# Optimization experiments

Measured on AMD Instinct MI355X. Metric: run time of the kernel, lower is better.

Reference implementation:

```python
import jax, jax.numpy as jnp
from jax import lax
import numpy as np


def conv2d(x, w, pad):
    # x: NCHW, w: OIHW
    return lax.conv_general_dilated(x, w, (1, 1), [(pad, pad), (pad, pad)],
                                    dimension_numbers=("NCHW", "OIHW", "NCHW"))


def make_dct_dict(num_atoms, num_dims):
    i = np.arange(num_atoms)[:, None].astype(np.float64)
    n = np.arange(num_dims)[None, :].astype(np.float64)
    w = np.cos((2.0 * n + 1.0) * i * (np.pi / (2.0 * num_dims)))
    w = w / np.linalg.norm(w, axis=1, keepdims=True)
    return jnp.asarray(w.T, dtype=jnp.float32)  # [num_dims, num_atoms]


def setup_inputs() -> dict:
    key = jax.random.key(0)
    B, C, H, W = 8, 64, 64, 64      # C = num_dims
    A = 256                          # num_atoms
    ks = jax.random.split(key, 10)
    s = 0.05
    Dict = make_dct_dict(A, C)       # [C, A]
    L = jnp.sum(Dict ** 2)           # ||Dict||_F^2 (scalar parameter)
    return {
        "x": jax.random.normal(ks[0], (B, C, H, W), jnp.float32),
        "conv_w": jax.random.normal(ks[1], (A, C, 3, 3), jnp.float32) * s,
        "conv_b": jax.random.normal(ks[2], (A,), jnp.float32) * s,
        "res1_w1": jax.random.normal(ks[3], (A // 2, A, 3, 3), jnp.float32) * s,
        "res1_w2": jax.random.normal(ks[4], (A, A // 2, 1, 1), jnp.float32) * s,
        "res2_w1": jax.random.normal(ks[5], (A // 2, A, 3, 3), jnp.float32) * s,
        "res2_w2": jax.random.normal(ks[6], (A, A // 2, 1, 1), jnp.float32) * s,
        "ca_w1": jax.random.normal(ks[7], (A // 16, A), jnp.float32) * s,  # Linear(A, A//16)
        "ca_w2": jax.random.normal(ks[8], (A, A // 16), jnp.float32) * s,  # Linear(A//16, A)
        "sa_w": jax.random.normal(ks[9], (1, 2, 3, 3), jnp.float32) * s,
        "Dict": Dict,
        "L": L,
        "num_iters": 16,
    }


def reference(x, conv_w, conv_b, res1_w1, res1_w2, res2_w1, res2_w2,
              ca_w1, ca_w2, sa_w, Dict, L, num_iters):
    def res_block(h, w1, w2):
        t = conv2d(jax.nn.relu(h), w1, 1)
        t = conv2d(jax.nn.relu(t), w2, 0)
        return h + t

    l = conv2d(x, conv_w, 1) + conv_b[None, :, None, None]
    l = res_block(l, res1_w1, res1_w2)
    l = res_block(l, res2_w1, res2_w2)

    # CBAM: channel attention (shared MLP on avg/max pooled features)
    avg = jnp.mean(l, axis=(2, 3))  # [B, A]
    mx = jnp.max(l, axis=(2, 3))
    fc = lambda v: jax.nn.relu(v @ ca_w1.T) @ ca_w2.T
    l = l * jax.nn.sigmoid(fc(avg) + fc(mx))[:, :, None, None]
    # CBAM: spatial attention
    s2 = jnp.concatenate([jnp.mean(l, axis=1, keepdims=True),
                          jnp.max(l, axis=1, keepdims=True)], axis=1)  # [B,2,H,W]
    l = l * jax.nn.sigmoid(conv2d(s2, sa_w, 1))

    lam = jnp.transpose(l / L, (0, 2, 3, 1))   # [B,H,W,A] per-position thresholds
    xp = jnp.transpose(x, (0, 2, 3, 1))        # [B,H,W,C]

    A = Dict.shape[1]
    S = (jnp.eye(A, dtype=Dict.dtype) - (Dict.T @ Dict) / L).T  # [A,A]
    y = xp @ Dict                               # [B,H,W,A]
    yL = y / L

    soft = lambda v: jnp.sign(v) * jnp.maximum(jnp.abs(v) - lam, 0.0)

    z0 = soft(y)

    def step(z, _):
        return soft(z @ S + yL), None

    z, _ = lax.scan(step, z0, None, length=num_iters)
    x_recon = z @ Dict.T                        # [B,H,W,C]

    return (jnp.transpose(z, (0, 3, 1, 2)),
            jnp.transpose(x_recon, (0, 3, 1, 2)),
            Dict)
```

## Files before the change

### kernel.cpp

```cpp
#include <hip/hip_runtime.h>
#include <hip/hip_bf16.h>

typedef __attribute__((ext_vector_type(8))) short short8v;
typedef __attribute__((ext_vector_type(4))) short short4v;
typedef __attribute__((ext_vector_type(4))) float float4v;

__device__ __forceinline__ unsigned short f2bu(float v){
  __hip_bfloat16 h = __float2bfloat16(v);
  union { __hip_bfloat16 h; unsigned short u; } cv; cv.h = h; return cv.u;
}

__device__ __forceinline__ float softt(float v, float lam){
  float t = fmaxf(fabsf(v) - lam, 0.f);
  float r = copysignf(t, v);
  return (v == 0.f) ? 0.f : r;
}

__global__ void k_Lin(const float* __restrict__ Lsrc, float* __restrict__ Lb){
  Lb[0] = Lsrc[0];
}

__global__ void k_gram(const float* __restrict__ D, unsigned short* __restrict__ Gb){
  int j = blockIdx.x, a = threadIdx.x;
  float acc = 0.f;
  for (int c = 0; c < 64; ++c)
    acc += D[c*256 + j] * D[c*256 + a];
  Gb[j*256 + a] = f2bu(acc);
}

__global__ void k_transpD(const float* __restrict__ D, float* __restrict__ DT,
                          unsigned short* __restrict__ DTb){
  int gid = blockIdx.x * 256 + threadIdx.x;
  if (gid < 16384) {
    int a = gid >> 6, c = gid & 63;
    float v = D[c*256 + a];
    DT[gid] = v;
    DTb[gid] = f2bu(v);
  }
}

__global__ void k_castw(const float* __restrict__ w, unsigned short* __restrict__ wb,
                        int n){
  int gid = blockIdx.x * 256 + threadIdx.x;
  if (gid < n) wb[gid] = f2bu(w[gid]);
}

__global__ void k_permw3(const float* __restrict__ w, unsigned short* __restrict__ wb,
                         int logI, int n){
  int gid = blockIdx.x * 256 + threadIdx.x;
  if (gid >= n) return;
  int I = 1 << logI;
  int i = gid & (I - 1);
  int t = gid >> logI;
  int o = t / 9;
  int r = t - o * 9;
  wb[gid] = f2bu(w[((o << logI) + i) * 9 + r]);
}

template<int KS, int CIN, bool BIAS, bool RES, bool WF32, bool WBF>
__global__ __launch_bounds__(256) void k_conv(
    const unsigned short* __restrict__ in, const unsigned short* __restrict__ wb,
    const float* __restrict__ bias, const float* res, float* outf,
    unsigned short* __restrict__ outb, int Cout)
{
  constexpr int NCH  = CIN / 32;
  constexpr int LNCH = (NCH == 2) ? 1 : (NCH == 4 ? 2 : 3);
  constexpr int K    = KS * KS * CIN;

  __shared__ unsigned short Asb[64][40];
  __shared__ unsigned short Bsb[128][40];

  const int tid = threadIdx.x;
  int bx = blockIdx.x;
  { const int cpx = gridDim.x >> 3; bx = (bx & 7) * cpx + (bx >> 3); }
  const int m0  = bx * 64;
  const int n0  = blockIdx.y * 128;
  const int b   = m0 >> 12;
  const int hw0 = m0 & 4095;
  const int h   = hw0 >> 6;
  const int w0  = hw0 & 63;

  const int sm  = tid & 63;
  const int sq8 = tid >> 6;
  const int bn  = tid & 127;
  const int bq  = tid >> 7;

  const int w   = tid >> 6;
  const int ln  = tid & 63;
  const int q   = ln >> 4;
  const int l16 = ln & 15;

  float4v acc[2][4];
  #pragma unroll
  for (int nt = 0; nt < 2; ++nt)
    #pragma unroll
    for (int mt = 0; mt < 4; ++mt)
      acc[nt][mt] = (float4v){0.f, 0.f, 0.f, 0.f};

  int sA = 0, sB = NCH;
  if (KS == 3) { sA = (h == 0 ? 3 : 0) * NCH; sB = (h == 63 ? 6 : 9) * NCH; }

  short8v a_r;
  short8v b_r0, b_r1;

  auto pref = [&](int s){
    const int r    = s >> LNCH;
    const int ccid = s & (NCH - 1);
    int hh = h, ww = w0 + sm;
    bool ok = true;
    if (KS == 3) {
      const int r3 = r / 3;
      const int dw = r - r3 * 3 - 1;
      hh = h + r3 - 1;
      ww += dw;
      ok = ((unsigned)ww < 64u);
    }
    a_r = (short8v){0,0,0,0,0,0,0,0};
    if (ok) {
      const unsigned short* ap = in +
          (((size_t)(b * CIN + ccid * 32 + sq8 * 8)) << 12) + (hh << 6) + ww;
      #pragma unroll
      for (int j = 0; j < 8; ++j)
        a_r[j] = (short)ap[(size_t)j << 12];
    }
    const unsigned short* bp = wb + (size_t)(n0 + bn) * K + s * 32 + bq * 16;
    b_r0 = *(const short8v*)(bp);
    b_r1 = *(const short8v*)(bp + 8);
  };

  pref(sA);
  for (int s = sA; s < sB; ) {
    *(short8v*)(&Asb[sm][sq8 * 8])      = a_r;
    *(short8v*)(&Bsb[bn][bq * 16])      = b_r0;
    *(short8v*)(&Bsb[bn][bq * 16 + 8])  = b_r1;
    __syncthreads();
    const int sn = s + 1;
    if (sn < sB) pref(sn);
    short8v Af[4];
    #pragma unroll
    for (int mt = 0; mt < 4; ++mt)
      Af[mt] = *(const short8v*)(&Asb[mt * 16 + l16][q * 8]);
    #pragma unroll
    for (int nt = 0; nt < 2; ++nt) {
      short8v Bf = *(const short8v*)(&Bsb[w * 32 + nt * 16 + l16][q * 8]);
      #pragma unroll
      for (int mt = 0; mt < 4; ++mt)
        acc[nt][mt] = __builtin_amdgcn_mfma_f32_16x16x32_bf16(
            Af[mt], Bf, acc[nt][mt], 0, 0, 0);
    }
    __syncthreads();
    s = sn;
  }

  #pragma unroll
  for (int nt = 0; nt < 2; ++nt) {
    const int n = n0 + w * 32 + nt * 16 + l16;
    float bv = 0.f;
    if (BIAS) bv = bias[n];
    #pragma unroll
    for (int mt = 0; mt < 4; ++mt) {
      const size_t base = (((size_t)(b * Cout + n)) << 12) + hw0 + mt * 16 + q * 4;
      float o[4];
      #pragma unroll
      for (int r2 = 0; r2 < 4; ++r2) o[r2] = acc[nt][mt][r2] + bv;
      if (RES) {
        float4 r4 = *(const float4*)(res + base);
        o[0] += r4.x; o[1] += r4.y; o[2] += r4.z; o[3] += r4.w;
      }
      if (WF32) {
        float4 o4; o4.x = o[0]; o4.y = o[1]; o4.z = o[2]; o4.w = o[3];
        *(float4*)(outf + base) = o4;
      }
      if (WBF) {
        short4v s4;
        #pragma unroll
        for (int r2 = 0; r2 < 4; ++r2) s4[r2] = (short)f2bu(fmaxf(o[r2], 0.f));
        *(short4v*)(outb + base) = s4;
      }
    }
  }
}

__global__ void k_pool(const float* __restrict__ l, float* __restrict__ avg,
                       float* __restrict__ mx){
  int b = blockIdx.y, a = blockIdx.x, tid = threadIdx.x;
  const float* p = l + ((size_t)(b * 256 + a) << 12);
  float s = 0.f, m = -1e30f;
  for (int i = tid; i < 4096; i += 256) { float v = p[i]; s += v; m = fmaxf(m, v); }
  __shared__ float ss[256], sm[256];
  ss[tid] = s; sm[tid] = m; __syncthreads();
  for (int o = 128; o > 0; o >>= 1) {
    if (tid < o) { ss[tid] += ss[tid+o]; sm[tid] = fmaxf(sm[tid], sm[tid+o]); }
    __syncthreads();
  }
  if (tid == 0) { avg[b*256+a] = ss[0] * (1.f/4096.f); mx[b*256+a] = sm[0]; }
}

__global__ void k_ca(const float* __restrict__ avg, const float* __restrict__ mx,
                     const float* __restrict__ w1, const float* __restrict__ w2,
                     float* __restrict__ cscale){
  int b = blockIdx.x, tid = threadIdx.x;
  __shared__ float h[16];
  if (tid < 16) {
    float sa = 0.f, sm = 0.f;
    for (int a = 0; a < 256; ++a) {
      float w = w1[tid*256 + a];
      sa += avg[b*256 + a] * w;
      sm += mx[b*256 + a] * w;
    }
    h[tid] = fmaxf(sa, 0.f) + fmaxf(sm, 0.f);
  }
  __syncthreads();
  float s = 0.f;
  for (int j = 0; j < 16; ++j) s += h[j] * w2[tid*16 + j];
  cscale[b*256 + tid] = 1.f / (1.f + __expf(-s));
}

__global__ void k_s2(const float* __restrict__ l, const float* __restrict__ cscale,
                     float* __restrict__ s2){
  int b = blockIdx.y;
  int hw = blockIdx.x * 256 + threadIdx.x;
  const float* p  = l + (((size_t)b * 256) << 12) + hw;
  const float* cs = cscale + b * 256;
  float s = 0.f, m = -1e30f;
  for (int a = 0; a < 256; ++a) {
    float v = p[(size_t)a << 12] * cs[a];
    s += v; m = fmaxf(m, v);
  }
  s2[((b*2) << 12) + hw]   = s * (1.f/256.f);
  s2[((b*2+1) << 12) + hw] = m;
}

__global__ void k_sa(const float* __restrict__ s2, const float* __restrict__ w,
                     float* __restrict__ sa){
  int b = blockIdx.y;
  int hw = blockIdx.x * 256 + threadIdx.x;
  int h = hw >> 6, ww = hw & 63;
  float acc = 0.f;
  for (int ch = 0; ch < 2; ++ch)
    for (int dh = -1; dh <= 1; ++dh)
      for (int dw = -1; dw <= 1; ++dw) {
        int hh = h + dh, wc = ww + dw;
        if ((unsigned)hh < 64u && (unsigned)wc < 64u)
          acc += s2[((b*2+ch) << 12) + (hh << 6) + wc] * w[ch*9 + (dh+1)*3 + (dw+1)];
      }
  sa[(b << 12) + hw] = 1.f / (1.f + __expf(-acc));
}

#define XTS 80

__device__ __forceinline__ int zoff(int pos, int au8){
  return pos * 256 + (((au8 ^ (pos & 15)) & 31) << 3);
}

__global__ __launch_bounds__(256, 2) void k_lista(
    const unsigned short* __restrict__ xb,
    const unsigned short* __restrict__ DTb,
    const unsigned short* __restrict__ Gb,
    const float* __restrict__ lmap, const float* __restrict__ csc,
    const float* __restrict__ sav, const float* __restrict__ Lb,
    float* __restrict__ zout)
{
  __shared__ unsigned short zbuf[2][16 * 256];

  const int tid = threadIdx.x;
  const int m0  = blockIdx.x * 16;
  const int b   = m0 >> 12;
  const int hw0 = m0 & 4095;
  const float invL = 1.0f / Lb[0];

  unsigned short* xTb = &zbuf[1][0];
  {
    const int i  = tid & 15;
    const int c0 = tid >> 4;
    #pragma unroll
    for (int cc = 0; cc < 4; ++cc) {
      int c = c0 + cc * 16;
      xTb[i * XTS + c] = xb[((b * 64 + c) << 12) + hw0 + i];
    }
  }

  const int w   = tid >> 6;
  const int ln  = tid & 63;
  const int q   = ln >> 4;
  const int l16 = ln & 15;

  short8v Sg[4][8];
  #pragma unroll
  for (int at = 0; at < 4; ++at)
    #pragma unroll
    for (int ks = 0; ks < 8; ++ks)
      Sg[at][ks] = *(const short8v*)(
          Gb + (size_t)(w * 64 + at * 16 + l16) * 256 + ks * 32 + q * 8);

  __syncthreads();

  float z[4][4], yl[4][4], lamr[4][4];

  {
    const short8v B0 = *(const short8v*)(&xTb[l16 * XTS + q * 8]);
    const short8v B1 = *(const short8v*)(&xTb[l16 * XTS + 32 + q * 8]);
    #pragma unroll
    for (int at = 0; at < 4; ++at) {
      const int abase = w * 64 + at * 16;
      const short8v A0 = *(const short8v*)(DTb + (abase + l16) * 64 + q * 8);
      const short8v A1 = *(const short8v*)(DTb + (abase + l16) * 64 + 32 + q * 8);
      float4v a = {0.f, 0.f, 0.f, 0.f};
      a = __builtin_amdgcn_mfma_f32_16x16x32_bf16(A0, B0, a, 0, 0, 0);
      a = __builtin_amdgcn_mfma_f32_16x16x32_bf16(A1, B1, a, 0, 0, 0);
      short4v pk;
      #pragma unroll
      for (int r = 0; r < 4; ++r) {
        const int atom = abase + q * 4 + r;
        const float lv = lmap[(((size_t)(b * 256 + atom)) << 12) + hw0 + l16];
        const float sv = sav[(b << 12) + hw0 + l16];
        const float cv = csc[b * 256 + atom];
        const float lm = ((lv * cv) * sv) * invL;
        const float yv = a[r];
        lamr[at][r] = lm;
        yl[at][r]   = yv * invL;
        const float z0 = softt(yv, lm);
        z[at][r] = z0;
        pk[r] = (short)f2bu(z0);
      }
      *(short4v*)(&zbuf[0][zoff(l16, w * 8 + at * 2 + (q >> 1)) + (q & 1) * 4]) = pk;
    }
  }
  __syncthreads();

  int cur = 0;
  for (int it = 0; it < 16; ++it) {
    #pragma unroll
    for (int at = 0; at < 4; ++at)
      #pragma unroll
      for (int ks = 0; ks < 8; ++ks)
        asm volatile("" : "+v"(Sg[at][ks]));

    float4v acc[4];
    #pragma unroll
    for (int at = 0; at < 4; ++at)
      acc[at] = (float4v){0.f, 0.f, 0.f, 0.f};

    #pragma unroll
    for (int ks = 0; ks < 8; ++ks) {
      const short8v B = *(const short8v*)(&zbuf[cur][zoff(l16, ks * 4 + q)]);
      acc[0] = __builtin_amdgcn_mfma_f32_16x16x32_bf16(Sg[0][ks], B, acc[0], 0, 0, 0);
      acc[1] = __builtin_amdgcn_mfma_f32_16x16x32_bf16(Sg[1][ks], B, acc[1], 0, 0, 0);
      acc[2] = __builtin_amdgcn_mfma_f32_16x16x32_bf16(Sg[2][ks], B, acc[2], 0, 0, 0);
      acc[3] = __builtin_amdgcn_mfma_f32_16x16x32_bf16(Sg[3][ks], B, acc[3], 0, 0, 0);
    }

    #pragma unroll
    for (int at = 0; at < 4; ++at) {
      short4v pk;
      #pragma unroll
      for (int r = 0; r < 4; ++r) {
        const float u  = fmaf(-invL, acc[at][r], z[at][r] + yl[at][r]);
        const float nz = softt(u, lamr[at][r]);
        z[at][r] = nz;
        pk[r] = (short)f2bu(nz);
      }
      *(short4v*)(&zbuf[cur ^ 1][zoff(l16, w * 8 + at * 2 + (q >> 1)) + (q & 1) * 4]) = pk;
    }
    __syncthreads();
    cur ^= 1;
  }

  #pragma unroll
  for (int at = 0; at < 4; ++at) {
    float4 o;
    o.x = z[at][0]; o.y = z[at][1]; o.z = z[at][2]; o.w = z[at][3];
    *(float4*)(&zout[(size_t)(m0 + l16) * 256 + w * 64 + at * 16 + q * 4]) = o;
  }
}

__global__ __launch_bounds__(256) void k_recon_simple(
    const float* __restrict__ z, const float* __restrict__ DT,
    float* __restrict__ out1)
{
  __shared__ float zs[16][256];
  const int tid = threadIdx.x;
  const int r0  = blockIdx.x * 16;
  const int b   = r0 >> 12;
  const int hw0 = r0 & 4095;

  for (int idx = tid; idx < 4096; idx += 256) {
    int r = idx >> 8, k = idx & 255;
    zs[r][k] = z[(r0 + r) * 256 + k];
  }
  __syncthreads();

  const int c  = tid & 63;
  const int rg = tid >> 6;
  float acc[4] = {0.f, 0.f, 0.f, 0.f};
  for (int a = 0; a < 256; ++a) {
    float d = DT[a * 64 + c];
    #pragma unroll
    for (int i = 0; i < 4; ++i) acc[i] += zs[rg + 4*i][a] * d;
  }
  #pragma unroll
  for (int i = 0; i < 4; ++i) {
    int r = rg + 4*i;
    out1[((b * 64 + c) << 12) + hw0 + r] = acc[i];
  }
}

__global__ __launch_bounds__(256) void k_zout_t(const float* __restrict__ z,
                                                float* __restrict__ out0){
  __shared__ float zs[64][65];
  const int tid = threadIdx.x;
  const int hwt = blockIdx.x * 64;
  const int at  = blockIdx.y * 64;
  const int b   = blockIdx.z;
  const int j   = tid & 63;
  const int i0  = tid >> 6;
  #pragma unroll
  for (int k = 0; k < 16; ++k) {
    int i = i0 + k * 4;
    zs[i][j] = z[(size_t)(b * 4096 + hwt + i) * 256 + at + j];
  }
  __syncthreads();
  #pragma unroll
  for (int k = 0; k < 16; ++k) {
    int i = i0 + k * 4;
    out0[(((size_t)(b * 256 + at + i)) << 12) + hwt + j] = zs[j][i];
  }
}

__global__ void k_dictout_f32(const float* __restrict__ D, float* __restrict__ out2){
  int i = blockIdx.x * 256 + threadIdx.x;
  if (i < 16384) out2[i] = D[i];
}

extern "C" void kernel_launch(void* const* d_in, const int* in_sizes, int n_in,
                              void* d_out, int out_size, void* d_ws, size_t ws_size,
                              hipStream_t stream)
{
  (void)in_sizes; (void)n_in; (void)out_size; (void)ws_size;

  const float* x    = (const float*)d_in[0];
  const float* cw   = (const float*)d_in[1];
  const float* cb   = (const float*)d_in[2];
  const float* r1w1 = (const float*)d_in[3];
  const float* r1w2 = (const float*)d_in[4];
  const float* r2w1 = (const float*)d_in[5];
  const float* r2w2 = (const float*)d_in[6];
  const float* caw1 = (const float*)d_in[7];
  const float* caw2 = (const float*)d_in[8];
  const float* saw  = (const float*)d_in[9];
  const float* D    = (const float*)d_in[10];
  const float* Lsrc = (const float*)d_in[11];

  float* p = (float*)d_ws;
  float* DT   = p; p += 16384;
  float* Lb   = p; p += 8;
  unsigned short* Gb  = (unsigned short*)p; p += 32768;
  unsigned short* DTb = (unsigned short*)p; p += 8192;
  unsigned short* cwb   = (unsigned short*)p; p += 73728;
  unsigned short* r1w1b = (unsigned short*)p; p += 147456;
  unsigned short* r1w2b = (unsigned short*)p; p += 16384;
  unsigned short* r2w1b = (unsigned short*)p; p += 147456;
  unsigned short* r2w2b = (unsigned short*)p; p += 16384;
  float* avg  = p; p += 2048;
  float* mx   = p; p += 2048;
  float* csc  = p; p += 2048;
  float* s2   = p; p += 65536;
  float* sa   = p; p += 32768;
  float* l    = p; p += 8388608;
  float* scr  = p; p += 8388608;
  float* zt   = p; p += 8388608;
  float* z    = zt;

  unsigned short* xb = (unsigned short*)scr;
  unsigned short* lb = (unsigned short*)(scr + 1048576);
  unsigned short* tb = (unsigned short*)(scr + 1048576 + 4194304);

  float* out0 = (float*)d_out;
  float* out1 = out0 + (size_t)8*256*4096;
  float* out2 = out1 + (size_t)8*64*4096;

  dim3 b256(256);

  k_Lin<<<dim3(1), dim3(1), 0, stream>>>(Lsrc, Lb);
  k_gram<<<dim3(256), b256, 0, stream>>>(D, Gb);
  k_transpD<<<dim3(64), b256, 0, stream>>>(D, DT, DTb);
  k_permw3<<<dim3(576),  b256, 0, stream>>>(cw,   cwb,   6, 147456);
  k_permw3<<<dim3(1152), b256, 0, stream>>>(r1w1, r1w1b, 8, 294912);
  k_castw <<<dim3(128),  b256, 0, stream>>>(r1w2, r1w2b, 32768);
  k_permw3<<<dim3(1152), b256, 0, stream>>>(r2w1, r2w1b, 8, 294912);
  k_castw <<<dim3(128),  b256, 0, stream>>>(r2w2, r2w2b, 32768);
  k_castw <<<dim3(8192), b256, 0, stream>>>(x, xb, 2097152);

  k_conv<3,  64, true,  false, true,  true ><<<dim3(512, 2), b256, 0, stream>>>(
      xb, cwb, cb, (const float*)nullptr, l, lb, 256);
  k_conv<3, 256, false, false, false, true ><<<dim3(512, 1), b256, 0, stream>>>(
      lb, r1w1b, (const float*)nullptr, (const float*)nullptr, (float*)nullptr, tb, 128);
  k_conv<1, 128, false, true,  true,  true ><<<dim3(512, 2), b256, 0, stream>>>(
      tb, r1w2b, (const float*)nullptr, l, l, lb, 256);
  k_conv<3, 256, false, false, false, true ><<<dim3(512, 1), b256, 0, stream>>>(
      lb, r2w1b, (const float*)nullptr, (const float*)nullptr, (float*)nullptr, tb, 128);
  k_conv<1, 128, false, true,  true,  false><<<dim3(512, 2), b256, 0, stream>>>(
      tb, r2w2b, (const float*)nullptr, l, l, (unsigned short*)nullptr, 256);

  k_pool<<<dim3(256, 8), b256, 0, stream>>>(l, avg, mx);
  k_ca<<<dim3(8), b256, 0, stream>>>(avg, mx, caw1, caw2, csc);
  k_s2<<<dim3(16, 8), b256, 0, stream>>>(l, csc, s2);
  k_sa<<<dim3(16, 8), b256, 0, stream>>>(s2, saw, sa);

  k_lista<<<dim3(2048), b256, 0, stream>>>(xb, DTb, Gb, l, csc, sa, Lb, z);

  k_recon_simple<<<dim3(2048), b256, 0, stream>>>(z, DT, out1);
  k_zout_t<<<dim3(64, 4, 8), b256, 0, stream>>>(z, out0);
  k_dictout_f32<<<dim3(64), b256, 0, stream>>>(D, out2);
}
```

Measured before the change: 479.0 us.

## Double conv K-tile to 64, raise LISTA occupancy, prioritize MFMA waves

The conv kernel now consumes 64 input channels per K-step instead of 32, which halves the number of barrier-synchronised iterations and doubles the MFMA work per shared-memory stage. Shared tiles grow to 72 columns. The LISTA kernel's launch bound moves from 2 to 4 blocks per SM, and its MFMA loop is wrapped in s_setprio so the matrix-issuing waves get scheduling priority. The trade-offs are more registers and LDS in the conv kernel, and possible register spills in LISTA under the tighter occupancy target, since it holds large Sg register arrays.

```diff
diff --git a/kernel.cpp b/kernel.cpp
--- a/kernel.cpp
+++ b/kernel.cpp
@@ -63,12 +63,11 @@
     const float* __restrict__ bias, const float* res, float* outf,
     unsigned short* __restrict__ outb, int Cout)
 {
-  constexpr int NCH  = CIN / 32;
-  constexpr int LNCH = (NCH == 2) ? 1 : (NCH == 4 ? 2 : 3);
-  constexpr int K    = KS * KS * CIN;
-
-  __shared__ unsigned short Asb[64][40];
-  __shared__ unsigned short Bsb[128][40];
+  constexpr int TPC = CIN / 64;
+  constexpr int K   = KS * KS * CIN;
+
+  __shared__ unsigned short Asb[64][72];
+  __shared__ unsigned short Bsb[128][72];
 
   const int tid = threadIdx.x;
   int bx = blockIdx.x;
@@ -97,15 +96,15 @@
     for (int mt = 0; mt < 4; ++mt)
       acc[nt][mt] = (float4v){0.f, 0.f, 0.f, 0.f};
 
-  int sA = 0, sB = NCH;
-  if (KS == 3) { sA = (h == 0 ? 3 : 0) * NCH; sB = (h == 63 ? 6 : 9) * NCH; }
-
-  short8v a_r;
-  short8v b_r0, b_r1;
+  int sA = 0, sB = TPC;
+  if (KS == 3) { sA = (h == 0 ? 3 : 0) * TPC; sB = (h == 63 ? 6 : 9) * TPC; }
+
+  short8v a_r0, a_r1;
+  short8v b_r0, b_r1, b_r2, b_r3;
 
   auto pref = [&](int s){
-    const int r    = s >> LNCH;
-    const int ccid = s & (NCH - 1);
+    const int r   = s / TPC;
+    const int c64 = s - r * TPC;
     int hh = h, ww = w0 + sm;
     bool ok = true;
     if (KS == 3) {
@@ -115,38 +114,54 @@
       ww += dw;
       ok = ((unsigned)ww < 64u);
     }
-    a_r = (short8v){0,0,0,0,0,0,0,0};
+    a_r0 = (short8v){0,0,0,0,0,0,0,0};
+    a_r1 = (short8v){0,0,0,0,0,0,0,0};
     if (ok) {
       const unsigned short* ap = in +
-          (((size_t)(b * CIN + ccid * 32 + sq8 * 8)) << 12) + (hh << 6) + ww;
+          (((size_t)(b * CIN + c64 * 64 + sq8 * 8)) << 12) + (hh << 6) + ww;
       #pragma unroll
       for (int j = 0; j < 8; ++j)
-        a_r[j] = (short)ap[(size_t)j << 12];
-    }
-    const unsigned short* bp = wb + (size_t)(n0 + bn) * K + s * 32 + bq * 16;
+        a_r0[j] = (short)ap[(size_t)j << 12];
+      const unsigned short* ap2 = ap + ((size_t)32 << 12);
+      #pragma unroll
+      for (int j = 0; j < 8; ++j)
+        a_r1[j] = (short)ap2[(size_t)j << 12];
+    }
+    const unsigned short* bp = wb + (size_t)(n0 + bn) * K + s * 64 + bq * 32;
     b_r0 = *(const short8v*)(bp);
     b_r1 = *(const short8v*)(bp + 8);
+    b_r2 = *(const short8v*)(bp + 16);
+    b_r3 = *(const short8v*)(bp + 24);
   };
 
   pref(sA);
   for (int s = sA; s < sB; ) {
-    *(short8v*)(&Asb[sm][sq8 * 8])      = a_r;
-    *(short8v*)(&Bsb[bn][bq * 16])      = b_r0;
-    *(short8v*)(&Bsb[bn][bq * 16 + 8])  = b_r1;
+    *(short8v*)(&Asb[sm][sq8 * 8])       = a_r0;
+    *(short8v*)(&Asb[sm][32 + sq8 * 8])  = a_r1;
+    *(short8v*)(&Bsb[bn][bq * 32])       = b_r0;
+    *(short8v*)(&Bsb[bn][bq * 32 + 8])   = b_r1;
+    *(short8v*)(&Bsb[bn][bq * 32 + 16])  = b_r2;
+    *(short8v*)(&Bsb[bn][bq * 32 + 24])  = b_r3;
     __syncthreads();
     const int sn = s + 1;
     if (sn < sB) pref(sn);
-    short8v Af[4];
-    #pragma unroll
-    for (int mt = 0; mt < 4; ++mt)
-      Af[mt] = *(const short8v*)(&Asb[mt * 16 + l16][q * 8]);
+    short8v Af[4][2];
+    #pragma unroll
+    for (int mt = 0; mt < 4; ++mt) {
+      Af[mt][0] = *(const short8v*)(&Asb[mt * 16 + l16][q * 8]);
+      Af[mt][1] = *(const short8v*)(&Asb[mt * 16 + l16][32 + q * 8]);
+    }
     #pragma unroll
     for (int nt = 0; nt < 2; ++nt) {
-      short8v Bf = *(const short8v*)(&Bsb[w * 32 + nt * 16 + l16][q * 8]);
-      #pragma unroll
-      for (int mt = 0; mt < 4; ++mt)
+      const short8v Bf0 = *(const short8v*)(&Bsb[w * 32 + nt * 16 + l16][q * 8]);
+      const short8v Bf1 = *(const short8v*)(&Bsb[w * 32 + nt * 16 + l16][32 + q * 8]);
+      #pragma unroll
+      for (int mt = 0; mt < 4; ++mt) {
         acc[nt][mt] = __builtin_amdgcn_mfma_f32_16x16x32_bf16(
-            Af[mt], Bf, acc[nt][mt], 0, 0, 0);
+            Af[mt][0], Bf0, acc[nt][mt], 0, 0, 0);
+        acc[nt][mt] = __builtin_amdgcn_mfma_f32_16x16x32_bf16(
+            Af[mt][1], Bf1, acc[nt][mt], 0, 0, 0);
+      }
     }
     __syncthreads();
     s = sn;
@@ -253,7 +268,7 @@
   return pos * 256 + (((au8 ^ (pos & 15)) & 31) << 3);
 }
 
-__global__ __launch_bounds__(256, 2) void k_lista(
+__global__ __launch_bounds__(256, 4) void k_lista(
     const unsigned short* __restrict__ xb,
     const unsigned short* __restrict__ DTb,
     const unsigned short* __restrict__ Gb,
@@ -341,6 +356,7 @@
     for (int at = 0; at < 4; ++at)
       acc[at] = (float4v){0.f, 0.f, 0.f, 0.f};
 
+    __builtin_amdgcn_s_setprio(1);
     #pragma unroll
     for (int ks = 0; ks < 8; ++ks) {
       const short8v B = *(const short8v*)(&zbuf[cur][zoff(l16, ks * 4 + q)]);
@@ -349,6 +365,7 @@
       acc[2] = __builtin_amdgcn_mfma_f32_16x16x32_bf16(Sg[2][ks], B, acc[2], 0, 0, 0);
       acc[3] = __builtin_amdgcn_mfma_f32_16x16x32_bf16(Sg[3][ks], B, acc[3], 0, 0, 0);
     }
+    __builtin_amdgcn_s_setprio(0);
 
     #pragma unroll
     for (int at = 0; at < 4; ++at) {
```

After: 1.791 ms. +273.9%, slower.
